# Kernel optimization log

Hardware: AMD Instinct MI355X
Metric: run time of the kernel (lower is better)

## Reference

```python
import jax, jax.numpy as jnp
import numpy as np

B, T, C, H = 4, 2048, 768, 12
HD = C // H
EPS = 1e-5

def _ln(x, s, b):
    m = jnp.mean(x, axis=-1, keepdims=True)
    v = jnp.mean(jnp.square(x - m), axis=-1, keepdims=True)
    return (x - m) * jax.lax.rsqrt(v + EPS) * s + b

def setup_inputs() -> dict:
    key = jax.random.key(0)
    ks = jax.random.split(key, 8)
    x = jax.random.normal(ks[0], (B, T, C), dtype=jnp.float32)
    mask = jnp.tril(jnp.ones((T, T), dtype=bool))[None, None, :, :]  # causal [1,1,T,T]
    s = lambda fan_in: 1.0 / np.sqrt(fan_in)
    return {
        "x": x,
        "mask": mask,
        "ln1_s": jnp.ones((C,), jnp.float32),
        "ln1_b": jnp.zeros((C,), jnp.float32),
        "w_attn": jax.random.normal(ks[1], (C, 3 * C), jnp.float32) * s(C),
        "b_attn": jnp.zeros((3 * C,), jnp.float32),
        "w_o": jax.random.normal(ks[2], (C, C), jnp.float32) * s(C),
        "b_o": jnp.zeros((C,), jnp.float32),
        "ln2_s": jnp.ones((C,), jnp.float32),
        "ln2_b": jnp.zeros((C,), jnp.float32),
        "w_fc": jax.random.normal(ks[3], (C, 4 * C), jnp.float32) * s(C),
        "b_fc": jnp.zeros((4 * C,), jnp.float32),
        "w_proj": jax.random.normal(ks[4], (4 * C, C), jnp.float32) * s(4 * C),
        "b_proj": jnp.zeros((C,), jnp.float32),
    }

def reference(x, mask, ln1_s, ln1_b, w_attn, b_attn, w_o, b_o,
              ln2_s, ln2_b, w_fc, b_fc, w_proj, b_proj):
    # --- attention branch (pre-LN) ---
    h = _ln(x, ln1_s, ln1_b)
    qkv = (h @ w_attn + b_attn).reshape(B, T, 3 * H, HD)
    q, k, v = jnp.array_split(qkv, 3, axis=2)  # each [B,T,H,HD]
    scale = 1.0 / jnp.sqrt(jnp.float32(HD))
    attn = jnp.einsum('bqhd,bkhd->bhqk', q, k) * scale
    attn = jnp.where(mask, attn, jnp.finfo(jnp.float32).min)
    attn = jax.nn.softmax(attn, axis=-1)
    ctx = jnp.einsum('bhqk,bkhd->bqhd', attn, v).reshape(B, T, C)
    x = x + ctx @ w_o + b_o
    # --- MLP branch (pre-LN) ---
    h = _ln(x, ln2_s, ln2_b)
    h = jax.nn.gelu(h @ w_fc + b_fc, approximate=True)
    x = x + h @ w_proj + b_proj
    return x
```

## Files before the change

kernel.cpp:

```cpp
#include <hip/hip_runtime.h>


typedef unsigned short u16;
typedef unsigned int u32;
typedef __attribute__((ext_vector_type(8))) short short8;
typedef __attribute__((ext_vector_type(4))) float f32x4;
typedef __attribute__((ext_vector_type(16))) float f32x16;

__device__ __forceinline__ u16 f2bf(float f) {
    union { float f; unsigned u; } v; v.f = f;
    unsigned u = v.u;
    unsigned r = (u + 0x7FFFu + ((u >> 16) & 1u)) >> 16;
    return (u16)r;
}

__device__ __forceinline__ u32 cvtpk_bf16(float lo, float hi) {
    u32 r;
    asm("v_cvt_pk_bf16_f32 %0, %1, %2" : "=v"(r) : "v"(lo), "v"(hi));
    return r;
}

__device__ __forceinline__ void gld16(const u16* g, u16* l) {
    __builtin_amdgcn_global_load_lds(
        (const __attribute__((address_space(1))) void*)g,
        (__attribute__((address_space(3))) void*)l, 16, 0, 0);
}

__device__ __forceinline__ float gelu_fast(float v) {
    float t = v * v;
    float z2n = v * (-2.3022078f - 0.10294376f * t);
    float e = __builtin_amdgcn_exp2f(z2n);
    return v * __builtin_amdgcn_rcpf(1.0f + e);
}

__global__ void transpose_bf16_kernel(const float* __restrict__ w,
                                      u16* __restrict__ wt, int K, int N) {
    __shared__ float t[32][33];
    int n0 = blockIdx.x * 32, k0 = blockIdx.y * 32;
    int tx = threadIdx.x, ty = threadIdx.y;
#pragma unroll
    for (int i = 0; i < 4; i++)
        t[ty + 8 * i][tx] = w[(size_t)(k0 + ty + 8 * i) * N + n0 + tx];
    __syncthreads();
#pragma unroll
    for (int i = 0; i < 4; i++)
        wt[(size_t)(n0 + ty + 8 * i) * K + k0 + tx] = f2bf(t[tx][ty + 8 * i]);
}

__global__ void ln_kernel(const float* __restrict__ x, const float* __restrict__ s,
                          const float* __restrict__ b, u16* __restrict__ out) {
    int row = blockIdx.x;
    int tid = threadIdx.x;
    const float* xr = x + (size_t)row * 768;
    float v0 = xr[tid], v1 = xr[tid + 256], v2 = xr[tid + 512];
    float sum = v0 + v1 + v2;
    float sq = v0 * v0 + v1 * v1 + v2 * v2;
#pragma unroll
    for (int off = 32; off; off >>= 1) {
        sum += __shfl_down(sum, off);
        sq += __shfl_down(sq, off);
    }
    __shared__ float red[8];
    int wid = tid >> 6, lane = tid & 63;
    if (lane == 0) { red[wid] = sum; red[4 + wid] = sq; }
    __syncthreads();
    if (tid == 0) {
        float s4 = red[0] + red[1] + red[2] + red[3];
        float q4 = red[4] + red[5] + red[6] + red[7];
        red[0] = s4 * (1.0f / 768.0f);
        red[1] = q4 * (1.0f / 768.0f);
    }
    __syncthreads();
    float mean = red[0];
    float var = red[1] - mean * mean;
    float rstd = rsqrtf(var + 1e-5f);
    u16* orow = out + (size_t)row * 768;
    orow[tid]       = f2bf((v0 - mean) * rstd * s[tid]       + b[tid]);
    orow[tid + 256] = f2bf((v1 - mean) * rstd * s[tid + 256] + b[tid + 256]);
    orow[tid + 512] = f2bf((v2 - mean) * rstd * s[tid + 512] + b[tid + 512]);
}

template <int GELU, int RES, int OUTMODE>
__global__ __launch_bounds__(256) void gemm_kernel(
    const u16* __restrict__ A, const u16* __restrict__ Wt,
    const float* __restrict__ bias, const float* __restrict__ res,
    void* __restrict__ out, int M, int N, int K,
    u16* __restrict__ qbuf, u16* __restrict__ kbuf, u16* __restrict__ vbuf) {
    __shared__ __align__(16) u16 lA[2][128 * 64];
    __shared__ __align__(16) u16 lB[2][128 * 64];
    int m0 = blockIdx.x * 128, n0 = blockIdx.y * 128;
    int tid = threadIdx.x;
    int wid = tid >> 6, lane = tid & 63;
    int wr = wid >> 1, wc = wid & 1;
    int l15 = lane & 15, lhi = lane >> 4;

    const u16* aptr[4];
    const u16* bptr[4];
#pragma unroll
    for (int s = 0; s < 4; s++) {
        int u = s * 256 + tid;
        int row = u >> 3;
        int c8 = (u & 7) ^ (row & 7);
        aptr[s] = A + (size_t)(m0 + row) * K + c8 * 8;
        bptr[s] = Wt + (size_t)(n0 + row) * K + c8 * 8;
    }

    f32x4 acc[4][4];
#pragma unroll
    for (int i = 0; i < 4; i++)
#pragma unroll
        for (int j = 0; j < 4; j++) acc[i][j] = (f32x4)0.0f;

#pragma unroll
    for (int s = 0; s < 4; s++) gld16(aptr[s], &lA[0][(s * 256 + tid) * 8]);
#pragma unroll
    for (int s = 0; s < 4; s++) gld16(bptr[s], &lB[0][(s * 256 + tid) * 8]);
    __syncthreads();

    int KT = K >> 6;
    int cur = 0;
    for (int t = 0; t < KT; t++) {
        if (t + 1 < KT) {
            int ko = (t + 1) << 6;
#pragma unroll
            for (int s = 0; s < 4; s++) gld16(aptr[s] + ko, &lA[cur ^ 1][(s * 256 + tid) * 8]);
#pragma unroll
            for (int s = 0; s < 4; s++) gld16(bptr[s] + ko, &lB[cur ^ 1][(s * 256 + tid) * 8]);
        }
        short8 af[2][4], bfr[2][4];
#pragma unroll
        for (int ks = 0; ks < 2; ks++)
#pragma unroll
            for (int f = 0; f < 4; f++) {
                int ra = wr * 64 + f * 16 + l15;
                af[ks][f] = *(const short8*)&lA[cur][ra * 64 + (((ks * 4 + lhi) ^ (ra & 7)) << 3)];
                int rb = wc * 64 + f * 16 + l15;
                bfr[ks][f] = *(const short8*)&lB[cur][rb * 64 + (((ks * 4 + lhi) ^ (rb & 7)) << 3)];
            }
#pragma unroll
        for (int ks = 0; ks < 2; ks++)
#pragma unroll
            for (int fm = 0; fm < 4; fm++)
#pragma unroll
                for (int fn = 0; fn < 4; fn++)
                    acc[fm][fn] = __builtin_amdgcn_mfma_f32_16x16x32_bf16(
                        af[ks][fm], bfr[ks][fn], acc[fm][fn], 0, 0, 0);
        __syncthreads();
        cur ^= 1;
    }

    if (OUTMODE == 2) {
        int region = n0 / 768;
#pragma unroll
        for (int fm = 0; fm < 4; fm++)
#pragma unroll
            for (int fn = 0; fn < 4; fn++) {
                int col = n0 + wc * 64 + fn * 16 + l15;
                float bv = bias[col];
                int c = col - region * 768;
                int h = c >> 6, d = c & 63;
#pragma unroll
                for (int r = 0; r < 4; r++) {
                    int row = m0 + wr * 64 + fm * 16 + lhi * 4 + r;
                    int bb = row >> 11, t = row & 2047;
                    u16 val = f2bf(acc[fm][fn][r] + bv);
                    size_t bh = (size_t)bb * 12 + h;
                    if (region == 0)      qbuf[(bh * 2048 + t) * 64 + d] = val;
                    else if (region == 1) kbuf[(bh * 2048 + t) * 64 + d] = val;
                    else                  vbuf[(bh * 64 + d) * 2048 + t] = val;
                }
            }
    } else {
#pragma unroll
        for (int fm = 0; fm < 4; fm++)
#pragma unroll
            for (int fn = 0; fn < 4; fn++) {
                int col = n0 + wc * 64 + fn * 16 + l15;
                float bv = bias[col];
#pragma unroll
                for (int r = 0; r < 4; r++) {
                    int row = m0 + wr * 64 + fm * 16 + lhi * 4 + r;
                    float v = acc[fm][fn][r] + bv;
                    if (RES) v += res[(size_t)row * N + col];
                    if (GELU) v = gelu_fast(v);
                    if (OUTMODE == 1)
                        ((u16*)out)[(size_t)row * N + col] = f2bf(v);
                    else
                        ((float*)out)[(size_t)row * N + col] = v;
                }
            }
    }
}

__global__ __launch_bounds__(256) void attn_kernel(const u16* __restrict__ qbuf,
                                                   const u16* __restrict__ kbuf,
                                                   const u16* __restrict__ vbuf,
                                                   u16* __restrict__ ctx) {
    int bid = blockIdx.x;
    int qt = 15 - (bid / 48);
    int bh = bid % 48;
    int b = bh / 12, h = bh % 12;
    int q0 = qt * 128;
    int tid = threadIdx.x, wid = tid >> 6, lane = tid & 63;
    int l31 = lane & 31, hi = lane >> 5;

    __shared__ __align__(16) u16 lK[2][64 * 64];
    __shared__ __align__(16) u16 lV[2][64 * 64];

    const size_t bhT = (size_t)bh * 2048;

    const u16* kp[2];
    const u16* vp[2];
#pragma unroll
    for (int s = 0; s < 2; s++) {
        int u = s * 256 + tid;
        int row = u >> 3;
        int c8 = (u & 7) ^ (row & 7);
        kp[s] = kbuf + (bhT + row) * 64 + c8 * 8;
        vp[s] = vbuf + ((size_t)bh * 64 + row) * 2048 + c8 * 8;
    }

    int qrow = q0 + wid * 32 + l31;
    short8 bq[4];
#pragma unroll
    for (int ks = 0; ks < 4; ks++)
        bq[ks] = *(const short8*)(qbuf + (bhT + qrow) * 64 + ks * 16 + hi * 8);

    f32x16 oacc[2];
#pragma unroll
    for (int dt = 0; dt < 2; dt++) oacc[dt] = (f32x16)0.0f;
    float mb = -1e30f, lr = 0.0f;
    const float C2 = 0.125f * 1.44269504089f;
    const float THR = 11.55f;
    int myq = q0 + wid * 32 + l31;
    int qmax = q0 + wid * 32 + 31;

    int nt = 2 * qt + 2;
#pragma unroll
    for (int s = 0; s < 2; s++) gld16(kp[s], &lK[0][(s * 256 + tid) * 8]);
#pragma unroll
    for (int s = 0; s < 2; s++) gld16(vp[s], &lV[0][(s * 256 + tid) * 8]);
    __syncthreads();

    int cur = 0;
    for (int t = 0; t < nt; t++) {
        int k0 = t * 64;
        if (t + 1 < nt) {
            int kn = (t + 1) * 64;
#pragma unroll
            for (int s = 0; s < 2; s++) gld16(kp[s] + (size_t)kn * 64, &lK[cur ^ 1][(s * 256 + tid) * 8]);
#pragma unroll
            for (int s = 0; s < 2; s++) gld16(vp[s] + kn, &lV[cur ^ 1][(s * 256 + tid) * 8]);
        }
        if (k0 <= qmax) {
            f32x16 sa[2];
#pragma unroll
            for (int kt = 0; kt < 2; kt++) sa[kt] = (f32x16)0.0f;
#pragma unroll
            for (int kt = 0; kt < 2; kt++) {
                int rk = kt * 32 + l31;
#pragma unroll
                for (int ks = 0; ks < 4; ks++) {
                    short8 ak = *(const short8*)&lK[cur][rk * 64 + (((ks * 2 + hi) ^ (rk & 7)) << 3)];
                    sa[kt] = __builtin_amdgcn_mfma_f32_32x32x16_bf16(ak, bq[ks], sa[kt], 0, 0, 0);
                }
            }
            if (k0 + 63 > q0 + wid * 32) {
#pragma unroll
                for (int kt = 0; kt < 2; kt++)
#pragma unroll
                    for (int r = 0; r < 16; r++) {
                        int key = k0 + kt * 32 + (r & 3) + 8 * (r >> 2) + 4 * hi;
                        if (key > myq) sa[kt][r] = -1e30f;
                    }
            }
            float tmax = -1e30f;
#pragma unroll
            for (int kt = 0; kt < 2; kt++)
#pragma unroll
                for (int r = 0; r < 16; r++) tmax = fmaxf(tmax, sa[kt][r]);
            tmax = fmaxf(tmax, __shfl_xor(tmax, 32));
            float tmb = tmax * C2;
            if (__any(tmb > mb + THR)) {
                float mbn = fmaxf(mb, tmb);
                float corr = __builtin_amdgcn_exp2f(mb - mbn);
#pragma unroll
                for (int r = 0; r < 16; r++) {
                    int qm = (r & 3) + 8 * (r >> 2) + 4 * hi;
                    float c = __shfl(corr, qm);
                    oacc[0][r] *= c;
                    oacc[1][r] *= c;
                }
                lr *= corr;
                mb = mbn;
            }
            float rs = 0.0f;
#pragma unroll
            for (int kt = 0; kt < 2; kt++)
#pragma unroll
                for (int r = 0; r < 16; r++) {
                    float pv = __builtin_amdgcn_exp2f(fmaf(sa[kt][r], C2, -mb));
                    sa[kt][r] = pv;
                    rs += pv;
                }
            rs += __shfl_xor(rs, 32);
            lr += rs;
            short8 pa[4];
#pragma unroll
            for (int kt = 0; kt < 2; kt++)
#pragma unroll
                for (int ks2 = 0; ks2 < 2; ks2++) {
                    int base = ks2 * 8;
                    u32 A0 = cvtpk_bf16(sa[kt][base + 0], sa[kt][base + 1]);
                    u32 B0 = cvtpk_bf16(sa[kt][base + 4], sa[kt][base + 5]);
                    u32 A1 = cvtpk_bf16(sa[kt][base + 2], sa[kt][base + 3]);
                    u32 B1 = cvtpk_bf16(sa[kt][base + 6], sa[kt][base + 7]);
                    u32 A0s = (u32)__shfl_xor((int)A0, 32);
                    u32 B0s = (u32)__shfl_xor((int)B0, 32);
                    u32 A1s = (u32)__shfl_xor((int)A1, 32);
                    u32 B1s = (u32)__shfl_xor((int)B1, 32);
                    union { u32 u[4]; short8 s; } w;
                    w.u[0] = hi ? B0s : A0;
                    w.u[1] = hi ? B1s : A1;
                    w.u[2] = hi ? B0 : A0s;
                    w.u[3] = hi ? B1 : A1s;
                    pa[kt * 2 + ks2] = w.s;
                }
#pragma unroll
            for (int kt = 0; kt < 2; kt++)
#pragma unroll
                for (int ks2 = 0; ks2 < 2; ks2++) {
                    short8 ap = pa[kt * 2 + ks2];
#pragma unroll
                    for (int dt = 0; dt < 2; dt++) {
                        int rd = dt * 32 + l31;
                        short8 bv = *(const short8*)&lV[cur][rd * 64 + (((kt * 4 + ks2 * 2 + hi) ^ (rd & 7)) << 3)];
                        oacc[dt] = __builtin_amdgcn_mfma_f32_32x32x16_bf16(ap, bv, oacc[dt], 0, 0, 0);
                    }
                }
        }
        __syncthreads();
        cur ^= 1;
    }
    const size_t rowb = (size_t)b * 2048;
    float inv = 1.0f / lr;
#pragma unroll
    for (int r = 0; r < 16; r++) {
        int qm = (r & 3) + 8 * (r >> 2) + 4 * hi;
        float ir = __shfl(inv, qm);
        int row = q0 + wid * 32 + qm;
        u16* op = ctx + (rowb + row) * 768 + h * 64 + l31;
        op[0]  = f2bf(oacc[0][r] * ir);
        op[32] = f2bf(oacc[1][r] * ir);
    }
}

extern "C" void kernel_launch(void* const* d_in, const int* in_sizes, int n_in,
                              void* d_out, int out_size, void* d_ws, size_t ws_size,
                              hipStream_t stream) {
    const float* x      = (const float*)d_in[0];
    const float* ln1_s  = (const float*)d_in[2];
    const float* ln1_b  = (const float*)d_in[3];
    const float* w_attn = (const float*)d_in[4];
    const float* b_attn = (const float*)d_in[5];
    const float* w_o    = (const float*)d_in[6];
    const float* b_o    = (const float*)d_in[7];
    const float* ln2_s  = (const float*)d_in[8];
    const float* ln2_b  = (const float*)d_in[9];
    const float* w_fc   = (const float*)d_in[10];
    const float* b_fc   = (const float*)d_in[11];
    const float* w_proj = (const float*)d_in[12];
    const float* b_proj = (const float*)d_in[13];

    char* ws = (char*)d_ws;
    u16* wT_attn = (u16*)(ws + 0);
    u16* wT_o    = (u16*)(ws + 3538944);
    u16* wT_fc   = (u16*)(ws + 4718592);
    u16* wT_proj = (u16*)(ws + 9437184);
    u16* bufA    = (u16*)(ws + 14155776);
    u16* qbuf    = (u16*)(ws + 26738688);
    u16* kbuf    = (u16*)(ws + 39321600);
    u16* vbuf    = (u16*)(ws + 51904512);
    u16* act     = (u16*)(ws + 26738688);
    float* x1    = (float*)(ws + 77070336);

    dim3 tb(32, 8);
    transpose_bf16_kernel<<<dim3(2304 / 32, 768 / 32), tb, 0, stream>>>(w_attn, wT_attn, 768, 2304);
    transpose_bf16_kernel<<<dim3(768 / 32, 768 / 32), tb, 0, stream>>>(w_o, wT_o, 768, 768);
    transpose_bf16_kernel<<<dim3(3072 / 32, 768 / 32), tb, 0, stream>>>(w_fc, wT_fc, 768, 3072);
    transpose_bf16_kernel<<<dim3(768 / 32, 3072 / 32), tb, 0, stream>>>(w_proj, wT_proj, 3072, 768);

    ln_kernel<<<8192, 256, 0, stream>>>(x, ln1_s, ln1_b, bufA);
    gemm_kernel<0, 0, 2><<<dim3(64, 18), 256, 0, stream>>>(bufA, wT_attn, b_attn, nullptr, nullptr,
                                                           8192, 2304, 768, qbuf, kbuf, vbuf);
    attn_kernel<<<768, 256, 0, stream>>>(qbuf, kbuf, vbuf, bufA);
    gemm_kernel<0, 1, 0><<<dim3(64, 6), 256, 0, stream>>>(bufA, wT_o, b_o, x, x1,
                                                          8192, 768, 768, nullptr, nullptr, nullptr);
    ln_kernel<<<8192, 256, 0, stream>>>(x1, ln2_s, ln2_b, bufA);
    gemm_kernel<1, 0, 1><<<dim3(64, 24), 256, 0, stream>>>(bufA, wT_fc, b_fc, nullptr, act,
                                                           8192, 3072, 768, nullptr, nullptr, nullptr);
    gemm_kernel<0, 1, 0><<<dim3(64, 6), 256, 0, stream>>>(act, wT_proj, b_proj, x1, (float*)d_out,
                                                          8192, 768, 3072, nullptr, nullptr, nullptr);
}
```

Measured before the change: 263.0 us.

## Fuse weight transposes, use 64-row tiles for narrow GEMMs, MFMA row sums in attention

Merges the four weight-transpose launches into one kernel indexed by tile. Adds a BM template parameter so the two N=768 GEMMs use 64-row tiles, doubling their grid from 384 to 768 blocks to fill the GPU better. In attention, the softmax row sum now comes from an extra MFMA against a ones vector instead of scalar adds and shuffles. The MFMA sections are wrapped in s_setprio hints. The extra MFMA adds matrix work, and smaller tiles reduce data reuse per block.

```diff
diff --git a/kernel.cpp b/kernel.cpp
--- a/kernel.cpp
+++ b/kernel.cpp
@@ -33,10 +33,20 @@
     return v * __builtin_amdgcn_rcpf(1.0f + e);
 }
 
-__global__ void transpose_bf16_kernel(const float* __restrict__ w,
-                                      u16* __restrict__ wt, int K, int N) {
+__global__ void transpose_all_kernel(const float* __restrict__ w_attn, u16* __restrict__ wT_attn,
+                                     const float* __restrict__ w_o,    u16* __restrict__ wT_o,
+                                     const float* __restrict__ w_fc,   u16* __restrict__ wT_fc,
+                                     const float* __restrict__ w_proj, u16* __restrict__ wT_proj) {
     __shared__ float t[32][33];
-    int n0 = blockIdx.x * 32, k0 = blockIdx.y * 32;
+    int tile = blockIdx.x;
+    const float* w; u16* wt; int N; int idx;
+    if (tile < 1728)      { w = w_attn; wt = wT_attn; N = 2304; idx = tile; }
+    else if (tile < 2304) { w = w_o;    wt = wT_o;    N = 768;  idx = tile - 1728; }
+    else if (tile < 4608) { w = w_fc;   wt = wT_fc;   N = 3072; idx = tile - 2304; }
+    else                  { w = w_proj; wt = wT_proj; N = 768;  idx = tile - 4608; }
+    int K = (tile >= 4608) ? 3072 : 768;
+    int nx = N / 32;
+    int n0 = (idx % nx) * 32, k0 = (idx / nx) * 32;
     int tx = threadIdx.x, ty = threadIdx.y;
 #pragma unroll
     for (int i = 0; i < 4; i++)
@@ -80,39 +90,48 @@
     orow[tid + 512] = f2bf((v2 - mean) * rstd * s[tid + 512] + b[tid + 512]);
 }
 
-template <int GELU, int RES, int OUTMODE>
+template <int GELU, int RES, int OUTMODE, int BM>
 __global__ __launch_bounds__(256) void gemm_kernel(
     const u16* __restrict__ A, const u16* __restrict__ Wt,
     const float* __restrict__ bias, const float* __restrict__ res,
     void* __restrict__ out, int M, int N, int K,
     u16* __restrict__ qbuf, u16* __restrict__ kbuf, u16* __restrict__ vbuf) {
-    __shared__ __align__(16) u16 lA[2][128 * 64];
+    constexpr int FM = BM / 32;
+    constexpr int SA = BM / 32;
+    constexpr int WR = BM / 2;
+    __shared__ __align__(16) u16 lA[2][BM * 64];
     __shared__ __align__(16) u16 lB[2][128 * 64];
-    int m0 = blockIdx.x * 128, n0 = blockIdx.y * 128;
+    int m0 = blockIdx.x * BM, n0 = blockIdx.y * 128;
     int tid = threadIdx.x;
     int wid = tid >> 6, lane = tid & 63;
     int wr = wid >> 1, wc = wid & 1;
     int l15 = lane & 15, lhi = lane >> 4;
 
-    const u16* aptr[4];
+    const u16* aptr[SA];
     const u16* bptr[4];
+#pragma unroll
+    for (int s = 0; s < SA; s++) {
+        int u = s * 256 + tid;
+        int row = u >> 3;
+        int c8 = (u & 7) ^ (row & 7);
+        aptr[s] = A + (size_t)(m0 + row) * K + c8 * 8;
+    }
 #pragma unroll
     for (int s = 0; s < 4; s++) {
         int u = s * 256 + tid;
         int row = u >> 3;
         int c8 = (u & 7) ^ (row & 7);
-        aptr[s] = A + (size_t)(m0 + row) * K + c8 * 8;
         bptr[s] = Wt + (size_t)(n0 + row) * K + c8 * 8;
     }
 
-    f32x4 acc[4][4];
-#pragma unroll
-    for (int i = 0; i < 4; i++)
+    f32x4 acc[FM][4];
+#pragma unroll
+    for (int i = 0; i < FM; i++)
 #pragma unroll
         for (int j = 0; j < 4; j++) acc[i][j] = (f32x4)0.0f;
 
 #pragma unroll
-    for (int s = 0; s < 4; s++) gld16(aptr[s], &lA[0][(s * 256 + tid) * 8]);
+    for (int s = 0; s < SA; s++) gld16(aptr[s], &lA[0][(s * 256 + tid) * 8]);
 #pragma unroll
     for (int s = 0; s < 4; s++) gld16(bptr[s], &lB[0][(s * 256 + tid) * 8]);
     __syncthreads();
@@ -123,24 +142,28 @@
         if (t + 1 < KT) {
             int ko = (t + 1) << 6;
 #pragma unroll
-            for (int s = 0; s < 4; s++) gld16(aptr[s] + ko, &lA[cur ^ 1][(s * 256 + tid) * 8]);
+            for (int s = 0; s < SA; s++) gld16(aptr[s] + ko, &lA[cur ^ 1][(s * 256 + tid) * 8]);
 #pragma unroll
             for (int s = 0; s < 4; s++) gld16(bptr[s] + ko, &lB[cur ^ 1][(s * 256 + tid) * 8]);
         }
-        short8 af[2][4], bfr[2][4];
-#pragma unroll
-        for (int ks = 0; ks < 2; ks++)
+        short8 af[2][FM], bfr[2][4];
+#pragma unroll
+        for (int ks = 0; ks < 2; ks++) {
+#pragma unroll
+            for (int f = 0; f < FM; f++) {
+                int ra = wr * WR + f * 16 + l15;
+                af[ks][f] = *(const short8*)&lA[cur][ra * 64 + (((ks * 4 + lhi) ^ (ra & 7)) << 3)];
+            }
 #pragma unroll
             for (int f = 0; f < 4; f++) {
-                int ra = wr * 64 + f * 16 + l15;
-                af[ks][f] = *(const short8*)&lA[cur][ra * 64 + (((ks * 4 + lhi) ^ (ra & 7)) << 3)];
                 int rb = wc * 64 + f * 16 + l15;
                 bfr[ks][f] = *(const short8*)&lB[cur][rb * 64 + (((ks * 4 + lhi) ^ (rb & 7)) << 3)];
             }
+        }
 #pragma unroll
         for (int ks = 0; ks < 2; ks++)
 #pragma unroll
-            for (int fm = 0; fm < 4; fm++)
+            for (int fm = 0; fm < FM; fm++)
 #pragma unroll
                 for (int fn = 0; fn < 4; fn++)
                     acc[fm][fn] = __builtin_amdgcn_mfma_f32_16x16x32_bf16(
@@ -152,7 +175,7 @@
     if (OUTMODE == 2) {
         int region = n0 / 768;
 #pragma unroll
-        for (int fm = 0; fm < 4; fm++)
+        for (int fm = 0; fm < FM; fm++)
 #pragma unroll
             for (int fn = 0; fn < 4; fn++) {
                 int col = n0 + wc * 64 + fn * 16 + l15;
@@ -161,7 +184,7 @@
                 int h = c >> 6, d = c & 63;
 #pragma unroll
                 for (int r = 0; r < 4; r++) {
-                    int row = m0 + wr * 64 + fm * 16 + lhi * 4 + r;
+                    int row = m0 + wr * WR + fm * 16 + lhi * 4 + r;
                     int bb = row >> 11, t = row & 2047;
                     u16 val = f2bf(acc[fm][fn][r] + bv);
                     size_t bh = (size_t)bb * 12 + h;
@@ -172,14 +195,14 @@
             }
     } else {
 #pragma unroll
-        for (int fm = 0; fm < 4; fm++)
+        for (int fm = 0; fm < FM; fm++)
 #pragma unroll
             for (int fn = 0; fn < 4; fn++) {
                 int col = n0 + wc * 64 + fn * 16 + l15;
                 float bv = bias[col];
 #pragma unroll
                 for (int r = 0; r < 4; r++) {
-                    int row = m0 + wr * 64 + fm * 16 + lhi * 4 + r;
+                    int row = m0 + wr * WR + fm * 16 + lhi * 4 + r;
                     float v = acc[fm][fn][r] + bv;
                     if (RES) v += res[(size_t)row * N + col];
                     if (GELU) v = gelu_fast(v);
@@ -226,10 +249,15 @@
     for (int ks = 0; ks < 4; ks++)
         bq[ks] = *(const short8*)(qbuf + (bhT + qrow) * 64 + ks * 16 + hi * 8);
 
-    f32x16 oacc[2];
+    short8 ones;
+#pragma unroll
+    for (int j = 0; j < 8; j++) ones[j] = (short)0x3F80;
+
+    f32x16 oacc[2], sacc;
 #pragma unroll
     for (int dt = 0; dt < 2; dt++) oacc[dt] = (f32x16)0.0f;
-    float mb = -1e30f, lr = 0.0f;
+    sacc = (f32x16)0.0f;
+    float mb = -1e30f;
     const float C2 = 0.125f * 1.44269504089f;
     const float THR = 11.55f;
     int myq = q0 + wid * 32 + l31;
@@ -256,6 +284,7 @@
             f32x16 sa[2];
 #pragma unroll
             for (int kt = 0; kt < 2; kt++) sa[kt] = (f32x16)0.0f;
+            __builtin_amdgcn_s_setprio(1);
 #pragma unroll
             for (int kt = 0; kt < 2; kt++) {
                 int rk = kt * 32 + l31;
@@ -265,6 +294,7 @@
                     sa[kt] = __builtin_amdgcn_mfma_f32_32x32x16_bf16(ak, bq[ks], sa[kt], 0, 0, 0);
                 }
             }
+            __builtin_amdgcn_s_setprio(0);
             if (k0 + 63 > q0 + wid * 32) {
 #pragma unroll
                 for (int kt = 0; kt < 2; kt++)
@@ -278,7 +308,8 @@
 #pragma unroll
             for (int kt = 0; kt < 2; kt++)
 #pragma unroll
-                for (int r = 0; r < 16; r++) tmax = fmaxf(tmax, sa[kt][r]);
+                for (int r = 0; r < 16; r += 2)
+                    tmax = fmaxf(tmax, fmaxf(sa[kt][r], sa[kt][r + 1]));
             tmax = fmaxf(tmax, __shfl_xor(tmax, 32));
             float tmb = tmax * C2;
             if (__any(tmb > mb + THR)) {
@@ -290,21 +321,15 @@
                     float c = __shfl(corr, qm);
                     oacc[0][r] *= c;
                     oacc[1][r] *= c;
-                }
-                lr *= corr;
+                    sacc[r] *= c;
+                }
                 mb = mbn;
             }
-            float rs = 0.0f;
 #pragma unroll
             for (int kt = 0; kt < 2; kt++)
 #pragma unroll
-                for (int r = 0; r < 16; r++) {
-                    float pv = __builtin_amdgcn_exp2f(fmaf(sa[kt][r], C2, -mb));
-                    sa[kt][r] = pv;
-                    rs += pv;
-                }
-            rs += __shfl_xor(rs, 32);
-            lr += rs;
+                for (int r = 0; r < 16; r++)
+                    sa[kt][r] = __builtin_amdgcn_exp2f(fmaf(sa[kt][r], C2, -mb));
             short8 pa[4];
 #pragma unroll
             for (int kt = 0; kt < 2; kt++)
@@ -326,6 +351,7 @@
                     w.u[3] = hi ? B1 : A1s;
                     pa[kt * 2 + ks2] = w.s;
                 }
+            __builtin_amdgcn_s_setprio(1);
 #pragma unroll
             for (int kt = 0; kt < 2; kt++)
 #pragma unroll
@@ -337,17 +363,18 @@
                         short8 bv = *(const short8*)&lV[cur][rd * 64 + (((kt * 4 + ks2 * 2 + hi) ^ (rd & 7)) << 3)];
                         oacc[dt] = __builtin_amdgcn_mfma_f32_32x32x16_bf16(ap, bv, oacc[dt], 0, 0, 0);
                     }
-                }
+                    sacc = __builtin_amdgcn_mfma_f32_32x32x16_bf16(ap, ones, sacc, 0, 0, 0);
+                }
+            __builtin_amdgcn_s_setprio(0);
         }
         __syncthreads();
         cur ^= 1;
     }
     const size_t rowb = (size_t)b * 2048;
-    float inv = 1.0f / lr;
 #pragma unroll
     for (int r = 0; r < 16; r++) {
+        float ir = __builtin_amdgcn_rcpf(sacc[r]);
         int qm = (r & 3) + 8 * (r >> 2) + 4 * hi;
-        float ir = __shfl(inv, qm);
         int row = q0 + wid * 32 + qm;
         u16* op = ctx + (rowb + row) * 768 + h * 64 + l31;
         op[0]  = f2bf(oacc[0][r] * ir);
@@ -384,21 +411,18 @@
     u16* act     = (u16*)(ws + 26738688);
     float* x1    = (float*)(ws + 77070336);
 
-    dim3 tb(32, 8);
-    transpose_bf16_kernel<<<dim3(2304 / 32, 768 / 32), tb, 0, stream>>>(w_attn, wT_attn, 768, 2304);
-    transpose_bf16_kernel<<<dim3(768 / 32, 768 / 32), tb, 0, stream>>>(w_o, wT_o, 768, 768);
-    transpose_bf16_kernel<<<dim3(3072 / 32, 768 / 32), tb, 0, stream>>>(w_fc, wT_fc, 768, 3072);
-    transpose_bf16_kernel<<<dim3(768 / 32, 3072 / 32), tb, 0, stream>>>(w_proj, wT_proj, 3072, 768);
+    transpose_all_kernel<<<6912, dim3(32, 8), 0, stream>>>(w_attn, wT_attn, w_o, wT_o,
+                                                           w_fc, wT_fc, w_proj, wT_proj);
 
     ln_kernel<<<8192, 256, 0, stream>>>(x, ln1_s, ln1_b, bufA);
-    gemm_kernel<0, 0, 2><<<dim3(64, 18), 256, 0, stream>>>(bufA, wT_attn, b_attn, nullptr, nullptr,
-                                                           8192, 2304, 768, qbuf, kbuf, vbuf);
+    gemm_kernel<0, 0, 2, 128><<<dim3(64, 18), 256, 0, stream>>>(bufA, wT_attn, b_attn, nullptr, nullptr,
+                                                                8192, 2304, 768, qbuf, kbuf, vbuf);
     attn_kernel<<<768, 256, 0, stream>>>(qbuf, kbuf, vbuf, bufA);
-    gemm_kernel<0, 1, 0><<<dim3(64, 6), 256, 0, stream>>>(bufA, wT_o, b_o, x, x1,
-                                                          8192, 768, 768, nullptr, nullptr, nullptr);
+    gemm_kernel<0, 1, 0, 64><<<dim3(128, 6), 256, 0, stream>>>(bufA, wT_o, b_o, x, x1,
+                                                               8192, 768, 768, nullptr, nullptr, nullptr);
     ln_kernel<<<8192, 256, 0, stream>>>(x1, ln2_s, ln2_b, bufA);
-    gemm_kernel<1, 0, 1><<<dim3(64, 24), 256, 0, stream>>>(bufA, wT_fc, b_fc, nullptr, act,
-                                                           8192, 3072, 768, nullptr, nullptr, nullptr);
-    gemm_kernel<0, 1, 0><<<dim3(64, 6), 256, 0, stream>>>(act, wT_proj, b_proj, x1, (float*)d_out,
-                                                          8192, 768, 3072, nullptr, nullptr, nullptr);
-}
+    gemm_kernel<1, 0, 1, 128><<<dim3(64, 24), 256, 0, stream>>>(bufA, wT_fc, b_fc, nullptr, act,
+                                                                8192, 3072, 768, nullptr, nullptr, nullptr);
+    gemm_kernel<0, 1, 0, 64><<<dim3(128, 6), 256, 0, stream>>>(act, wT_proj, b_proj, x1, (float*)d_out,
+                                                               8192, 768, 3072, nullptr, nullptr, nullptr);
+}
```

Result: no change. 267.8 us (+1.8%).
